# Optimization experiments

Measured on AMD Instinct MI355X. Metric: run time of the kernel, lower is better.

Reference implementation:

```python
import jax, jax.numpy as jnp
import numpy as np

N = 50000      # number of nodes
D = 128        # embedding dim
K = 16         # padded neighbors per node
B = 100000     # number of train pairs
LAYERS = 2     # convolution layers


def setup_inputs() -> dict:
    key = jax.random.key(0)
    k_pairs, k_lab, k_nbr, k_emb, k_w1, k_w2 = jax.random.split(key, 6)
    pairs = jax.random.randint(k_pairs, (B, 2), 0, N, dtype=jnp.int64 if jax.config.jax_enable_x64 else jnp.int32)
    labels = jax.random.randint(k_lab, (B,), 0, 2, dtype=jnp.int32)
    neighbors = jax.random.randint(k_nbr, (N, K), 0, N, dtype=jnp.int32)
    embedding = jax.random.normal(k_emb, (N, D), dtype=jnp.float32)
    W1 = jax.random.normal(k_w1, (2 * D, D), dtype=jnp.float32) * (1.0 / np.sqrt(2 * D))
    b1 = jnp.zeros((D,), dtype=jnp.float32)
    W2 = jax.random.normal(k_w2, (D, 2), dtype=jnp.float32) * (1.0 / np.sqrt(D))
    b2 = jnp.zeros((2,), dtype=jnp.float32)
    return {"pairs": pairs, "labels": labels, "neighbors": neighbors,
            "embedding": embedding, "W1": W1, "b1": b1, "W2": W2, "b2": b2}


def _aggregate(embedding, neighbors):
    # Multi-layer mean neighbor aggregation over all N nodes.
    H = embedding
    for _ in range(LAYERS):
        # gather [N, K, D] then mean over neighbors -> [N, D]
        H = jnp.take(H, neighbors, axis=0).mean(axis=1)
    return H


def reference(pairs, labels, neighbors, embedding, W1, b1, W2, b2):
    H = _aggregate(embedding, neighbors)           # [N, D]
    src = jnp.take(H, pairs[:, 0], axis=0)         # [B, D]
    dst = jnp.take(H, pairs[:, 1], axis=0)         # [B, D]
    x = jnp.concatenate([src, dst], axis=-1)       # [B, 2D]
    h = jax.nn.relu(x @ W1 + b1)                   # [B, D]
    logits = h @ W2 + b2                           # [B, 2]
    # Original applies Softmax, then CrossEntropyLoss (which log_softmaxes again).
    probs = jax.nn.softmax(logits, axis=-1)
    logp = jax.nn.log_softmax(probs, axis=-1)
    loss = -jnp.take_along_axis(logp, labels[:, None].astype(jnp.int32), axis=1).mean()
    return loss
```

## Files before the change

### kernel.cpp

```cpp
#include <hip/hip_runtime.h>
#include <hip/hip_bf16.h>

#define NNODES 50000
#define DIM    128
#define KNBR   16
#define NPAIRS 100000
#define PBLK   1250
#define PITER  5

typedef float          f32x4  __attribute__((ext_vector_type(4)));
typedef float          f32x2  __attribute__((ext_vector_type(2)));
typedef __bf16         bf16x8 __attribute__((ext_vector_type(8)));
typedef unsigned short u16x8  __attribute__((ext_vector_type(8)));
typedef unsigned int   u32x2  __attribute__((ext_vector_type(2)));

__device__ __forceinline__ unsigned short f2bf(float f) {
    unsigned int u = __builtin_bit_cast(unsigned int, f);
    u = (u + 0x7fffu + ((u >> 16) & 1u)) >> 16;
    return (unsigned short)u;
}

#if __has_builtin(__builtin_amdgcn_cvt_pk_f32_fp8) && __has_builtin(__builtin_amdgcn_cvt_pk_fp8_f32)
template <bool HI>
__device__ __forceinline__ f32x2 fp8x2_dec(unsigned int w) {
    return __builtin_amdgcn_cvt_pk_f32_fp8((int)w, HI);
}
template <bool HI>
__device__ __forceinline__ unsigned int fp8x2_enc(float a, float b, unsigned int old) {
    return (unsigned int)__builtin_amdgcn_cvt_pk_fp8_f32(a, b, (int)old, HI);
}
#else
__device__ __forceinline__ float e4m3_dec1(unsigned int b) {
    unsigned int s = (b & 0x80u) << 24;
    unsigned int em = b & 0x7fu;
    float mag = (em >= 8u)
        ? __builtin_bit_cast(float, (((em >> 3) + 120u) << 23) | ((em & 7u) << 20))
        : (float)em * 0.001953125f;
    return __builtin_bit_cast(float, __builtin_bit_cast(unsigned int, mag) | s);
}
template <bool HI>
__device__ __forceinline__ f32x2 fp8x2_dec(unsigned int w) {
    unsigned int v = HI ? (w >> 16) : w;
    f32x2 r; r[0] = e4m3_dec1(v & 0xffu); r[1] = e4m3_dec1((v >> 8) & 0xffu);
    return r;
}
__device__ __forceinline__ unsigned int e4m3_enc1(float f) {
    unsigned int s = (__builtin_bit_cast(unsigned int, f) >> 24) & 0x80u;
    float af = fminf(fabsf(f), 448.0f);
    unsigned int u = __builtin_bit_cast(unsigned int, af);
    int e = (int)(u >> 23) - 127;
    if (e < -9) return s;
    if (e < -6) { int q = (int)rintf(af * 512.0f); return s | (unsigned int)q; }
    unsigned int mant = u & 0x7fffffu;
    unsigned int r = (mant + 0x7ffffu + ((mant >> 20) & 1u)) >> 20;
    unsigned int out = (((unsigned int)(e + 7)) << 3) + r;
    if (out > 0x7eu) out = 0x7eu;
    return s | out;
}
template <bool HI>
__device__ __forceinline__ unsigned int fp8x2_enc(float a, float b, unsigned int old) {
    unsigned int p = e4m3_enc1(a) | (e4m3_enc1(b) << 8);
    return HI ? ((old & 0x0000ffffu) | (p << 16)) : ((old & 0xffff0000u) | p);
}
#endif

#define AS1 __attribute__((address_space(1)))
#define AS3 __attribute__((address_space(3)))
__device__ __forceinline__ void gload_lds16(const void* g, void* l) {
    __builtin_amdgcn_global_load_lds((AS1 void*)(g), (AS3 void*)(l), 16, 0, 0);
}

__global__ void w1t_kernel(const float* __restrict__ W1, unsigned short* __restrict__ W1t,
                           float* __restrict__ out) {
    int g = blockIdx.x * 256 + threadIdx.x;
    int i = g >> 7;
    int d = g & 127;
    W1t[d * 256 + i] = f2bf(W1[g]);
    if (g == 0) out[0] = 0.f;
}

__global__ void e2f8_kernel(const float* __restrict__ E, unsigned int* __restrict__ E8) {
    int g = blockIdx.x * 256 + threadIdx.x;
    const f32x4 v0 = *(const f32x4*)(E + (size_t)g * 8);
    const f32x4 v1 = *(const f32x4*)(E + (size_t)g * 8 + 4);
    unsigned int w0 = 0, w1 = 0;
    w0 = fp8x2_enc<false>(v0[0], v0[1], w0);
    w0 = fp8x2_enc<true >(v0[2], v0[3], w0);
    w1 = fp8x2_enc<false>(v1[0], v1[1], w1);
    w1 = fp8x2_enc<true >(v1[2], v1[3], w1);
    u32x2 o; o[0] = w0; o[1] = w1;
    *(u32x2*)(E8 + (size_t)g * 2) = o;
}

__device__ __forceinline__ void agg_core(const unsigned char* __restrict__ T,
                                         const int* __restrict__ nbr,
                                         unsigned char* lds_wave,
                                         int node_base, int lane, float* a) {
    const int rsub = lane >> 3;
    const int bcol = (lane & 7) * 16;
    const int* nb = nbr + node_base * KNBR;
#pragma unroll
    for (int i = 0; i < 8; ++i) {
        int nl = nb[i * 8 + rsub];
        gload_lds16(T + (size_t)nl * 128 + bcol, lds_wave + i * 1024);
    }
    asm volatile("s_waitcnt vmcnt(0)" ::: "memory");
    __builtin_amdgcn_sched_barrier(0);
    const int g = lane >> 4;
    const int c = lane & 15;
#pragma unroll
    for (int j = 0; j < 8; ++j) a[j] = 0.f;
#pragma unroll
    for (int k = 0; k < KNBR; ++k) {
        const u32x2 v = *(const u32x2*)(lds_wave + (g * 16 + k) * 128 + c * 8);
        f32x2 f;
        f = fp8x2_dec<false>(v[0]); a[0] += f[0]; a[1] += f[1];
        f = fp8x2_dec<true >(v[0]); a[2] += f[0]; a[3] += f[1];
        f = fp8x2_dec<false>(v[1]); a[4] += f[0]; a[5] += f[1];
        f = fp8x2_dec<true >(v[1]); a[6] += f[0]; a[7] += f[1];
    }
}

__global__ __launch_bounds__(256) void agg1_kernel(const unsigned char* __restrict__ E8,
                                                   const int* __restrict__ nbr,
                                                   unsigned char* __restrict__ H1f8) {
    __shared__ unsigned char SL[4][8192];
    const int t = threadIdx.x, wave = t >> 6, lane = t & 63;
    const int node_base = blockIdx.x * 16 + wave * 4;
    float a[8];
    agg_core(E8, nbr, SL[wave], node_base, lane, a);
    const int g = lane >> 4, c = lane & 15;
    unsigned int o0 = 0, o1 = 0;
    o0 = fp8x2_enc<false>(a[0] * 0.0625f, a[1] * 0.0625f, o0);
    o0 = fp8x2_enc<true >(a[2] * 0.0625f, a[3] * 0.0625f, o0);
    o1 = fp8x2_enc<false>(a[4] * 0.0625f, a[5] * 0.0625f, o1);
    o1 = fp8x2_enc<true >(a[6] * 0.0625f, a[7] * 0.0625f, o1);
    u32x2 o; o[0] = o0; o[1] = o1;
    *(u32x2*)(H1f8 + (size_t)(node_base + g) * 128 + c * 8) = o;
}

__global__ __launch_bounds__(256) void agg2_kernel(const unsigned char* __restrict__ H1f8,
                                                   const int* __restrict__ nbr,
                                                   unsigned short* __restrict__ H2b) {
    __shared__ unsigned char SL[4][8192];
    const int t = threadIdx.x, wave = t >> 6, lane = t & 63;
    const int node_base = blockIdx.x * 16 + wave * 4;
    float a[8];
    agg_core(H1f8, nbr, SL[wave], node_base, lane, a);
    const int g = lane >> 4, c = lane & 15;
    u16x8 o;
#pragma unroll
    for (int j = 0; j < 8; ++j) o[j] = f2bf(a[j] * 0.0625f);
    *(u16x8*)(H2b + (size_t)(node_base + g) * DIM + c * 8) = o;
}

__global__ __launch_bounds__(256, 2) void gemmpq_kernel(
    const unsigned short* __restrict__ H2b, const unsigned short* __restrict__ W1t,
    unsigned short* __restrict__ PQb) {
    __shared__ unsigned char  Ast[64 * 256];
    __shared__ unsigned short Cbuf[64 * 256];

    const int tid = threadIdx.x, wave = tid >> 6, lane = tid & 63;
    const int lg = lane >> 4, ll = lane & 15;
    const int rowbase = blockIdx.x * 64;

    {
        const int lq = (lane & 15) * 16;
        const int lr = lane >> 4;
#pragma unroll
        for (int i = 0; i < 4; ++i) {
            int r0 = wave * 16 + i * 4;
            int row = r0 + lr;
            int grow = rowbase + row; if (grow >= NNODES) grow = NNODES - 1;
            int b = lq ^ ((row & 7) << 4);
            gload_lds16((const char*)H2b + (size_t)grow * 256 + b, Ast + r0 * 256);
        }
    }

    const int qoff = (wave >= 2) ? 256 : 0;
    bf16x8 breg[4][4];
#pragma unroll
    for (int cg = 0; cg < 4; ++cg) {
        int jj = (wave * 64 + cg * 16 + ll) & 127;
#pragma unroll
        for (int ks = 0; ks < 4; ++ks)
            breg[cg][ks] = *(const bf16x8*)((const char*)W1t + jj * 512 + qoff + ks * 64 + lg * 16);
    }
    __syncthreads();

    f32x4 acc[4][4];
    {
        f32x4 z = {0.f, 0.f, 0.f, 0.f};
#pragma unroll
        for (int i = 0; i < 4; ++i)
#pragma unroll
            for (int j = 0; j < 4; ++j) acc[i][j] = z;
    }
#pragma unroll
    for (int ks = 0; ks < 4; ++ks) {
#pragma unroll
        for (int mf = 0; mf < 4; ++mf) {
            int row = mf * 16 + ll;
            bf16x8 af = *(const bf16x8*)(Ast + row * 256 + ((ks * 64 + lg * 16) ^ ((row & 7) << 4)));
#pragma unroll
            for (int cg = 0; cg < 4; ++cg)
                acc[mf][cg] = __builtin_amdgcn_mfma_f32_16x16x32_bf16(af, breg[cg][ks], acc[mf][cg], 0, 0, 0);
        }
    }

#pragma unroll
    for (int mf = 0; mf < 4; ++mf)
#pragma unroll
        for (int cg = 0; cg < 4; ++cg) {
            int col = wave * 64 + cg * 16 + ll;
#pragma unroll
            for (int r = 0; r < 4; ++r)
                Cbuf[(mf * 16 + lg * 4 + r) * 256 + col] = f2bf(acc[mf][cg][r]);
        }
    __syncthreads();
#pragma unroll
    for (int it = 0; it < 8; ++it) {
        int c = tid + it * 256;
        int row = c >> 5, cw = c & 31;
        int grow = rowbase + row;
        if (grow < NNODES)
            *(u16x8*)((char*)PQb + (size_t)grow * 512 + cw * 16) =
                *(const u16x8*)((const char*)Cbuf + row * 512 + cw * 16);
    }
}

__global__ __launch_bounds__(256) void pair_loss_kernel(
    const int* __restrict__ pairs, const int* __restrict__ labels,
    const unsigned short* __restrict__ PQb, const float* __restrict__ b1,
    const float* __restrict__ W2, const float* __restrict__ b2,
    float* __restrict__ out) {
    __shared__ float sred[4];
    const int tid = threadIdx.x, wave = tid >> 6, lane = tid & 63;
    const int pg = lane >> 4, c = lane & 15;

    float b1c[8], w2a[8], w2b[8];
#pragma unroll
    for (int j = 0; j < 8; ++j) {
        b1c[j] = b1[c * 8 + j];
        w2a[j] = W2[(c * 8 + j) * 2];
        w2b[j] = W2[(c * 8 + j) * 2 + 1];
    }
    const float b20 = b2[0], b21 = b2[1];

    float lacc = 0.f;
#pragma unroll
    for (int it = 0; it < PITER; ++it) {
        int p = (blockIdx.x + it * PBLK) * 16 + wave * 4 + pg;
        int s = pairs[p * 2], d = pairs[p * 2 + 1];
        bf16x8 pb = *(const bf16x8*)((const char*)PQb + (size_t)s * 512 + c * 16);
        bf16x8 qb = *(const bf16x8*)((const char*)PQb + (size_t)d * 512 + 256 + c * 16);
        float l0 = 0.f, l1 = 0.f;
#pragma unroll
        for (int j = 0; j < 8; ++j) {
            float h = fmaxf((float)pb[j] + (float)qb[j] + b1c[j], 0.f);
            l0 += h * w2a[j];
            l1 += h * w2b[j];
        }
#pragma unroll
        for (int sdist = 1; sdist < 16; sdist <<= 1) {
            l0 += __shfl_xor(l0, sdist, 16);
            l1 += __shfl_xor(l1, sdist, 16);
        }
        if (c == 0) {
            l0 += b20; l1 += b21;
            float mx = fmaxf(l0, l1);
            float e0 = __expf(l0 - mx), e1 = __expf(l1 - mx);
            float inv = 1.f / (e0 + e1);
            float q0 = e0 * inv, q1 = e1 * inv;
            float lse2 = __logf(__expf(q0) + __expf(q1));
            lacc += lse2 - (labels[p] ? q1 : q0);
        }
    }
#pragma unroll
    for (int sdist = 1; sdist < 64; sdist <<= 1) lacc += __shfl_xor(lacc, sdist, 64);
    if (lane == 0) sred[wave] = lacc;
    __syncthreads();
    if (tid == 0)
        atomicAdd(out, (sred[0] + sred[1] + sred[2] + sred[3]) * (1.0f / (float)NPAIRS));
}

extern "C" void kernel_launch(void* const* d_in, const int* in_sizes, int n_in,
                              void* d_out, int out_size, void* d_ws, size_t ws_size,
                              hipStream_t stream) {
    const int*   pairs  = (const int*)d_in[0];
    const int*   labels = (const int*)d_in[1];
    const int*   nbr    = (const int*)d_in[2];
    const float* E      = (const float*)d_in[3];
    const float* W1     = (const float*)d_in[4];
    const float* b1     = (const float*)d_in[5];
    const float* W2     = (const float*)d_in[6];
    const float* b2     = (const float*)d_in[7];
    float* out = (float*)d_out;

    char* ws = (char*)d_ws;
    unsigned short* W1t  = (unsigned short*)(ws);
    unsigned short* H2b  = (unsigned short*)(ws + 65536);
    unsigned char*  E8   = (unsigned char*)(ws + 65536 + 12800000);
    unsigned char*  H1f8 = E8 + 6400000;
    unsigned short* PQb  = (unsigned short*)E8;

    w1t_kernel<<<dim3(128), dim3(256), 0, stream>>>(W1, W1t, out);
    e2f8_kernel<<<dim3((NNODES * DIM) / (256 * 8)), dim3(256), 0, stream>>>(E, (unsigned int*)E8);
    agg1_kernel<<<dim3(NNODES / 16), dim3(256), 0, stream>>>(E8, nbr, H1f8);
    agg2_kernel<<<dim3(NNODES / 16), dim3(256), 0, stream>>>(H1f8, nbr, H2b);
    gemmpq_kernel<<<dim3((NNODES + 63) / 64), dim3(256), 0, stream>>>(H2b, W1t, PQb);
    pair_loss_kernel<<<dim3(PBLK), dim3(256), 0, stream>>>(pairs, labels, PQb, b1, W2, b2, out);
}
```

Before: 152.2 us.

## Quantize embeddings and hidden states to 4-bit, store PQ in fp8

Embedding and the first aggregation output now use a custom 4-bit sign-magnitude code (8 levels up to 6), halving gather traffic compared with fp8. The aggregation kernels drop the LDS staging and have each thread load 4-byte words from its 16 neighbours directly. The GEMM folds b1 into its output and writes P/Q as fp8, halving the random-gather bytes in the pair-loss kernel. The very coarse 4-bit quantization, with the first layer stored at a 4x scale, risks noticeably degrading loss accuracy.

```diff
diff --git a/kernel.cpp b/kernel.cpp
--- a/kernel.cpp
+++ b/kernel.cpp
@@ -18,6 +18,9 @@
     unsigned int u = __builtin_bit_cast(unsigned int, f);
     u = (u + 0x7fffu + ((u >> 16) & 1u)) >> 16;
     return (unsigned short)u;
+}
+__device__ __forceinline__ float bf2f(unsigned short u) {
+    return __builtin_bit_cast(float, (unsigned int)u << 16);
 }
 
 #if __has_builtin(__builtin_amdgcn_cvt_pk_f32_fp8) && __has_builtin(__builtin_amdgcn_cvt_pk_fp8_f32)
@@ -64,6 +67,20 @@
 }
 #endif
 
+__device__ __forceinline__ unsigned enc4(float x) {
+    float ax = fabsf(x);
+    unsigned m =
+        ax < 0.25f ? 0u : ax < 0.75f ? 1u : ax < 1.25f ? 2u : ax < 1.75f ? 3u :
+        ax < 2.5f  ? 4u : ax < 3.5f  ? 5u : ax < 5.0f  ? 6u : 7u;
+    return m | (x < 0.f ? 8u : 0u);
+}
+__device__ __forceinline__ float dec4(unsigned n) {
+    unsigned m = n & 7u;
+    float mag = (m < 2u) ? (float)m * 0.5f
+                         : (float)((m & 1u) + 2u) * 0.25f * (float)(1u << (m >> 1));
+    return (n & 8u) ? -mag : mag;
+}
+
 #define AS1 __attribute__((address_space(1)))
 #define AS3 __attribute__((address_space(3)))
 __device__ __forceinline__ void gload_lds16(const void* g, void* l) {
@@ -79,84 +96,67 @@
     if (g == 0) out[0] = 0.f;
 }
 
-__global__ void e2f8_kernel(const float* __restrict__ E, unsigned int* __restrict__ E8) {
+__global__ void e2f4_kernel(const float* __restrict__ E, unsigned int* __restrict__ E4) {
     int g = blockIdx.x * 256 + threadIdx.x;
     const f32x4 v0 = *(const f32x4*)(E + (size_t)g * 8);
     const f32x4 v1 = *(const f32x4*)(E + (size_t)g * 8 + 4);
-    unsigned int w0 = 0, w1 = 0;
-    w0 = fp8x2_enc<false>(v0[0], v0[1], w0);
-    w0 = fp8x2_enc<true >(v0[2], v0[3], w0);
-    w1 = fp8x2_enc<false>(v1[0], v1[1], w1);
-    w1 = fp8x2_enc<true >(v1[2], v1[3], w1);
-    u32x2 o; o[0] = w0; o[1] = w1;
-    *(u32x2*)(E8 + (size_t)g * 2) = o;
-}
-
-__device__ __forceinline__ void agg_core(const unsigned char* __restrict__ T,
-                                         const int* __restrict__ nbr,
-                                         unsigned char* lds_wave,
-                                         int node_base, int lane, float* a) {
-    const int rsub = lane >> 3;
-    const int bcol = (lane & 7) * 16;
-    const int* nb = nbr + node_base * KNBR;
-#pragma unroll
-    for (int i = 0; i < 8; ++i) {
-        int nl = nb[i * 8 + rsub];
-        gload_lds16(T + (size_t)nl * 128 + bcol, lds_wave + i * 1024);
-    }
-    asm volatile("s_waitcnt vmcnt(0)" ::: "memory");
-    __builtin_amdgcn_sched_barrier(0);
-    const int g = lane >> 4;
-    const int c = lane & 15;
-#pragma unroll
-    for (int j = 0; j < 8; ++j) a[j] = 0.f;
-#pragma unroll
-    for (int k = 0; k < KNBR; ++k) {
-        const u32x2 v = *(const u32x2*)(lds_wave + (g * 16 + k) * 128 + c * 8);
-        f32x2 f;
-        f = fp8x2_dec<false>(v[0]); a[0] += f[0]; a[1] += f[1];
-        f = fp8x2_dec<true >(v[0]); a[2] += f[0]; a[3] += f[1];
-        f = fp8x2_dec<false>(v[1]); a[4] += f[0]; a[5] += f[1];
-        f = fp8x2_dec<true >(v[1]); a[6] += f[0]; a[7] += f[1];
-    }
-}
-
-__global__ __launch_bounds__(256) void agg1_kernel(const unsigned char* __restrict__ E8,
+    unsigned w = 0;
+#pragma unroll
+    for (int j = 0; j < 4; ++j) w |= enc4(v0[j]) << (4 * j);
+#pragma unroll
+    for (int j = 0; j < 4; ++j) w |= enc4(v1[j]) << (16 + 4 * j);
+    E4[g] = w;
+}
+
+__global__ __launch_bounds__(256) void agg1_kernel(const unsigned char* __restrict__ E4,
                                                    const int* __restrict__ nbr,
-                                                   unsigned char* __restrict__ H1f8) {
-    __shared__ unsigned char SL[4][8192];
-    const int t = threadIdx.x, wave = t >> 6, lane = t & 63;
-    const int node_base = blockIdx.x * 16 + wave * 4;
-    float a[8];
-    agg_core(E8, nbr, SL[wave], node_base, lane, a);
-    const int g = lane >> 4, c = lane & 15;
-    unsigned int o0 = 0, o1 = 0;
-    o0 = fp8x2_enc<false>(a[0] * 0.0625f, a[1] * 0.0625f, o0);
-    o0 = fp8x2_enc<true >(a[2] * 0.0625f, a[3] * 0.0625f, o0);
-    o1 = fp8x2_enc<false>(a[4] * 0.0625f, a[5] * 0.0625f, o1);
-    o1 = fp8x2_enc<true >(a[6] * 0.0625f, a[7] * 0.0625f, o1);
-    u32x2 o; o[0] = o0; o[1] = o1;
-    *(u32x2*)(H1f8 + (size_t)(node_base + g) * 128 + c * 8) = o;
-}
-
-__global__ __launch_bounds__(256) void agg2_kernel(const unsigned char* __restrict__ H1f8,
+                                                   unsigned char* __restrict__ H14) {
+    const int t = threadIdx.x;
+    const int node = blockIdx.x * 16 + (t >> 4);
+    const int c = t & 15;
+    const int* nl = nbr + node * KNBR;
+    unsigned v[16];
+#pragma unroll
+    for (int k = 0; k < KNBR; ++k)
+        v[k] = *(const unsigned*)(E4 + (size_t)nl[k] * 64 + c * 4);
+    float a[8] = {0.f,0.f,0.f,0.f,0.f,0.f,0.f,0.f};
+#pragma unroll
+    for (int k = 0; k < KNBR; ++k)
+#pragma unroll
+        for (int j = 0; j < 8; ++j)
+            a[j] += dec4((v[k] >> (4 * j)) & 0xFu);
+    unsigned w = 0;
+#pragma unroll
+    for (int j = 0; j < 8; ++j) w |= enc4(a[j] * 0.25f) << (4 * j);
+    *(unsigned*)(H14 + (size_t)node * 64 + c * 4) = w;
+}
+
+__global__ __launch_bounds__(256) void agg2_kernel(const unsigned char* __restrict__ H14,
                                                    const int* __restrict__ nbr,
                                                    unsigned short* __restrict__ H2b) {
-    __shared__ unsigned char SL[4][8192];
-    const int t = threadIdx.x, wave = t >> 6, lane = t & 63;
-    const int node_base = blockIdx.x * 16 + wave * 4;
-    float a[8];
-    agg_core(H1f8, nbr, SL[wave], node_base, lane, a);
-    const int g = lane >> 4, c = lane & 15;
+    const int t = threadIdx.x;
+    const int node = blockIdx.x * 16 + (t >> 4);
+    const int c = t & 15;
+    const int* nl = nbr + node * KNBR;
+    unsigned v[16];
+#pragma unroll
+    for (int k = 0; k < KNBR; ++k)
+        v[k] = *(const unsigned*)(H14 + (size_t)nl[k] * 64 + c * 4);
+    float a[8] = {0.f,0.f,0.f,0.f,0.f,0.f,0.f,0.f};
+#pragma unroll
+    for (int k = 0; k < KNBR; ++k)
+#pragma unroll
+        for (int j = 0; j < 8; ++j)
+            a[j] += dec4((v[k] >> (4 * j)) & 0xFu);
     u16x8 o;
 #pragma unroll
-    for (int j = 0; j < 8; ++j) o[j] = f2bf(a[j] * 0.0625f);
-    *(u16x8*)(H2b + (size_t)(node_base + g) * DIM + c * 8) = o;
+    for (int j = 0; j < 8; ++j) o[j] = f2bf(a[j] * 0.015625f);
+    *(u16x8*)(H2b + (size_t)node * DIM + c * 8) = o;
 }
 
 __global__ __launch_bounds__(256, 2) void gemmpq_kernel(
     const unsigned short* __restrict__ H2b, const unsigned short* __restrict__ W1t,
-    unsigned short* __restrict__ PQb) {
+    const float* __restrict__ b1, unsigned char* __restrict__ PQ8) {
     __shared__ unsigned char  Ast[64 * 256];
     __shared__ unsigned short Cbuf[64 * 256];
 
@@ -179,9 +179,12 @@
 
     const int qoff = (wave >= 2) ? 256 : 0;
     bf16x8 breg[4][4];
+    float badd[4];
 #pragma unroll
     for (int cg = 0; cg < 4; ++cg) {
-        int jj = (wave * 64 + cg * 16 + ll) & 127;
+        int col = wave * 64 + cg * 16 + ll;
+        int jj = col & 127;
+        badd[cg] = (wave < 2) ? b1[col] : 0.f;
 #pragma unroll
         for (int ks = 0; ks < 4; ++ks)
             breg[cg][ks] = *(const bf16x8*)((const char*)W1t + jj * 512 + qoff + ks * 64 + lg * 16);
@@ -215,33 +218,39 @@
             int col = wave * 64 + cg * 16 + ll;
 #pragma unroll
             for (int r = 0; r < 4; ++r)
-                Cbuf[(mf * 16 + lg * 4 + r) * 256 + col] = f2bf(acc[mf][cg][r]);
+                Cbuf[(mf * 16 + lg * 4 + r) * 256 + col] = f2bf(acc[mf][cg][r] + badd[cg]);
         }
     __syncthreads();
+
 #pragma unroll
     for (int it = 0; it < 8; ++it) {
-        int c = tid + it * 256;
-        int row = c >> 5, cw = c & 31;
+        int cc = it * 256 + tid;
+        int row = cc >> 5, cw = cc & 31;
         int grow = rowbase + row;
-        if (grow < NNODES)
-            *(u16x8*)((char*)PQb + (size_t)grow * 512 + cw * 16) =
-                *(const u16x8*)((const char*)Cbuf + row * 512 + cw * 16);
+        if (grow < NNODES) {
+            const unsigned short* src = Cbuf + row * 256 + cw * 8;
+            unsigned w0 = 0, w1 = 0;
+            w0 = fp8x2_enc<false>(bf2f(src[0]), bf2f(src[1]), w0);
+            w0 = fp8x2_enc<true >(bf2f(src[2]), bf2f(src[3]), w0);
+            w1 = fp8x2_enc<false>(bf2f(src[4]), bf2f(src[5]), w1);
+            w1 = fp8x2_enc<true >(bf2f(src[6]), bf2f(src[7]), w1);
+            u32x2 o; o[0] = w0; o[1] = w1;
+            *(u32x2*)(PQ8 + (size_t)grow * 256 + cw * 8) = o;
+        }
     }
 }
 
 __global__ __launch_bounds__(256) void pair_loss_kernel(
     const int* __restrict__ pairs, const int* __restrict__ labels,
-    const unsigned short* __restrict__ PQb, const float* __restrict__ b1,
-    const float* __restrict__ W2, const float* __restrict__ b2,
-    float* __restrict__ out) {
+    const unsigned char* __restrict__ PQ8, const float* __restrict__ W2,
+    const float* __restrict__ b2, float* __restrict__ out) {
     __shared__ float sred[4];
     const int tid = threadIdx.x, wave = tid >> 6, lane = tid & 63;
     const int pg = lane >> 4, c = lane & 15;
 
-    float b1c[8], w2a[8], w2b[8];
+    float w2a[8], w2b[8];
 #pragma unroll
     for (int j = 0; j < 8; ++j) {
-        b1c[j] = b1[c * 8 + j];
         w2a[j] = W2[(c * 8 + j) * 2];
         w2b[j] = W2[(c * 8 + j) * 2 + 1];
     }
@@ -252,12 +261,18 @@
     for (int it = 0; it < PITER; ++it) {
         int p = (blockIdx.x + it * PBLK) * 16 + wave * 4 + pg;
         int s = pairs[p * 2], d = pairs[p * 2 + 1];
-        bf16x8 pb = *(const bf16x8*)((const char*)PQb + (size_t)s * 512 + c * 16);
-        bf16x8 qb = *(const bf16x8*)((const char*)PQb + (size_t)d * 512 + 256 + c * 16);
+        u32x2 pw = *(const u32x2*)(PQ8 + (size_t)s * 256 + c * 8);
+        u32x2 qw = *(const u32x2*)(PQ8 + (size_t)d * 256 + 128 + c * 8);
+        f32x2 pa = fp8x2_dec<false>(pw[0]), pb = fp8x2_dec<true>(pw[0]);
+        f32x2 pc_ = fp8x2_dec<false>(pw[1]), pd = fp8x2_dec<true>(pw[1]);
+        f32x2 qa = fp8x2_dec<false>(qw[0]), qb = fp8x2_dec<true>(qw[0]);
+        f32x2 qc = fp8x2_dec<false>(qw[1]), qd = fp8x2_dec<true>(qw[1]);
+        float pe[8] = {pa[0], pa[1], pb[0], pb[1], pc_[0], pc_[1], pd[0], pd[1]};
+        float qe[8] = {qa[0], qa[1], qb[0], qb[1], qc[0], qc[1], qd[0], qd[1]};
         float l0 = 0.f, l1 = 0.f;
 #pragma unroll
         for (int j = 0; j < 8; ++j) {
-            float h = fmaxf((float)pb[j] + (float)qb[j] + b1c[j], 0.f);
+            float h = fmaxf(pe[j] + qe[j], 0.f);
             l0 += h * w2a[j];
             l1 += h * w2b[j];
         }
@@ -298,16 +313,16 @@
     float* out = (float*)d_out;
 
     char* ws = (char*)d_ws;
-    unsigned short* W1t  = (unsigned short*)(ws);
-    unsigned short* H2b  = (unsigned short*)(ws + 65536);
-    unsigned char*  E8   = (unsigned char*)(ws + 65536 + 12800000);
-    unsigned char*  H1f8 = E8 + 6400000;
-    unsigned short* PQb  = (unsigned short*)E8;
+    unsigned short* W1t = (unsigned short*)(ws);
+    unsigned short* H2b = (unsigned short*)(ws + 65536);
+    unsigned char*  E4  = (unsigned char*)(ws + 65536 + 12800000);
+    unsigned char*  H14 = E4 + 3200000;
+    unsigned char*  PQ8 = H14 + 3200000;
 
     w1t_kernel<<<dim3(128), dim3(256), 0, stream>>>(W1, W1t, out);
-    e2f8_kernel<<<dim3((NNODES * DIM) / (256 * 8)), dim3(256), 0, stream>>>(E, (unsigned int*)E8);
-    agg1_kernel<<<dim3(NNODES / 16), dim3(256), 0, stream>>>(E8, nbr, H1f8);
-    agg2_kernel<<<dim3(NNODES / 16), dim3(256), 0, stream>>>(H1f8, nbr, H2b);
-    gemmpq_kernel<<<dim3((NNODES + 63) / 64), dim3(256), 0, stream>>>(H2b, W1t, PQb);
-    pair_loss_kernel<<<dim3(PBLK), dim3(256), 0, stream>>>(pairs, labels, PQb, b1, W2, b2, out);
-}
+    e2f4_kernel<<<dim3((NNODES * DIM) / (256 * 8)), dim3(256), 0, stream>>>(E, (unsigned int*)E4);
+    agg1_kernel<<<dim3(NNODES / 16), dim3(256), 0, stream>>>(E4, nbr, H14);
+    agg2_kernel<<<dim3(NNODES / 16), dim3(256), 0, stream>>>(H14, nbr, H2b);
+    gemmpq_kernel<<<dim3((NNODES + 63) / 64), dim3(256), 0, stream>>>(H2b, W1t, b1, PQ8);
+    pair_loss_kernel<<<dim3(PBLK), dim3(256), 0, stream>>>(pairs, labels, PQ8, W2, b2, out);
+}
```

Result: slower. 215.7 us (+41.7%).
